# Optimization experiments

Hardware: AMD Instinct MI355X
Metric: run time of the kernel (lower is better)

Reference implementation:

```python
import jax, jax.numpy as jnp
import numpy as np

B, T1, H, P, V = 4096, 65, 64, 50, 32
D = H + P  # input_size = 114


def setup_inputs() -> dict:
    key = jax.random.key(0)
    ks = jax.random.split(key, 20)
    s = 1.0 / np.sqrt(D)
    sh = 1.0 / np.sqrt(H)
    inp = {
        "phonetic_input": jax.random.normal(ks[0], (B, P), dtype=jnp.float32),
        "char_seq": jax.random.randint(ks[1], (B, T1), 0, V, dtype=jnp.int64),
        "emb": jax.random.normal(ks[2], (V, H), dtype=jnp.float32).at[0].set(0.0),  # padding_idx=0
        "W_rx": jax.random.uniform(ks[3], (D, H), jnp.float32, -s, s),
        "b_rx": jax.random.uniform(ks[4], (H,), jnp.float32, -s, s),
        "W_rh": jax.random.uniform(ks[5], (H, H), jnp.float32, -sh, sh),
        "b_rh": jax.random.uniform(ks[6], (H,), jnp.float32, -sh, sh),
        "W_zx": jax.random.uniform(ks[7], (D, H), jnp.float32, -s, s),
        "b_zx": jax.random.uniform(ks[8], (H,), jnp.float32, -s, s),
        "W_zh": jax.random.uniform(ks[9], (H, H), jnp.float32, -sh, sh),
        "b_zh": jax.random.uniform(ks[10], (H,), jnp.float32, -sh, sh),
        "W_hx": jax.random.uniform(ks[11], (D, H), jnp.float32, -s, s),
        "b_hx": jax.random.uniform(ks[12], (H,), jnp.float32, -s, s),
        "W_hh": jax.random.uniform(ks[13], (H, H), jnp.float32, -sh, sh),
        "b_hh": jax.random.uniform(ks[14], (H,), jnp.float32, -sh, sh),
        "W_proj": jax.random.uniform(ks[15], (H, V), jnp.float32, -sh, sh),
        "b_proj": jax.random.uniform(ks[16], (V,), jnp.float32, -sh, sh),
    }
    return inp


def reference(phonetic_input, char_seq, emb, W_rx, b_rx, W_rh, b_rh, W_zx, b_zx,
              W_zh, b_zh, W_hx, b_hx, W_hh, b_hh, W_proj, b_proj):
    input_seq = char_seq[:, :-1]          # [B, T]
    target_seq = char_seq[:, 1:]          # [B, T]
    Bsz, T = input_seq.shape

    char_emb = emb[input_seq]                                   # [B, T, H]
    phon = jnp.broadcast_to(phonetic_input[:, None, :], (Bsz, T, P))
    x = jnp.concatenate([char_emb, phon], axis=2)               # [B, T, D]

    # Hoist input-side projections into batched GEMMs, [T, B, H] for scan
    xr = jnp.einsum('btd,dh->tbh', x, W_rx) + b_rx
    xz = jnp.einsum('btd,dh->tbh', x, W_zx) + b_zx
    xh = jnp.einsum('btd,dh->tbh', x, W_hx) + b_hx

    h0 = jnp.zeros((Bsz, H), dtype=x.dtype)

    def step(h, inputs):
        xr_t, xz_t, xh_t = inputs
        r = jax.nn.sigmoid(xr_t + h @ W_rh + b_rh)
        z = jax.nn.sigmoid(xz_t + h @ W_zh + b_zh)
        c = jnp.tanh(xh_t + (r * h) @ W_hh + b_hh)
        h_new = (1.0 - z) * h + z * c
        return h_new, h_new

    _, hs = jax.lax.scan(step, h0, (xr, xz, xh))                # [T, B, H]
    logits = jnp.einsum('tbh,hv->btv', hs, W_proj) + b_proj     # [B, T, V]

    # cross_entropy with ignore_index=0 (mean over non-ignored)
    targets = target_seq.reshape(-1)
    logp = jax.nn.log_softmax(logits.reshape(-1, V), axis=-1)
    nll = -jnp.take_along_axis(logp, targets[:, None], axis=-1)[:, 0]
    mask = (targets != 0).astype(logits.dtype)
    loss = jnp.sum(nll * mask) / jnp.maximum(jnp.sum(mask), 1.0)
    return logits, loss
```

## Files before the change

### kernel.cpp

```cpp
#include <hip/hip_runtime.h>
#include <stdint.h>

#define Bsz 4096
#define Tn  64
#define T1n 65
#define Hn  64
#define Pn  50
#define Vn  32

typedef __attribute__((ext_vector_type(8))) short short8;
typedef __attribute__((ext_vector_type(4))) float floatx4;

__device__ __forceinline__ float bf2f(unsigned short u) {
  union { unsigned int i; float f; } x; x.i = ((unsigned int)u) << 16; return x.f;
}
__device__ __forceinline__ unsigned short f2bf(float f) {
  union { float f; unsigned int i; } x; x.f = f;
  return (unsigned short)((x.i + 0x7FFFu + ((x.i >> 16) & 1u)) >> 16);
}
__device__ __forceinline__ float fast_sigmoid(float x) {
  return __builtin_amdgcn_rcpf(1.f + __expf(-x));
}
__device__ __forceinline__ float fast_tanh(float x) {
  return 1.f - 2.f * __builtin_amdgcn_rcpf(1.f + __expf(2.f * x));
}

__device__ __forceinline__ short8 load_bfrag(const float* __restrict__ W, int ncols, int col, int kbase) {
  short8 f;
#pragma unroll
  for (int j = 0; j < 8; ++j) f[j] = (short)f2bf(W[(long)(kbase + j) * ncols + col]);
  return f;
}

__launch_bounds__(512)
__global__ void gru_kernel(const float* __restrict__ phon,
                           const int* __restrict__ cs,
                           const float* __restrict__ emb,
                           const float* __restrict__ Wrx, const float* __restrict__ brx,
                           const float* __restrict__ Wrh, const float* __restrict__ brh,
                           const float* __restrict__ Wzx, const float* __restrict__ bzx,
                           const float* __restrict__ Wzh, const float* __restrict__ bzh,
                           const float* __restrict__ Whx, const float* __restrict__ bhx,
                           const float* __restrict__ Whh, const float* __restrict__ bhh,
                           const float* __restrict__ Wpj, const float* __restrict__ bpj_g,
                           float* __restrict__ ws,
                           float* __restrict__ outp) {
  __shared__ unsigned short tbl_s[3 * 32 * 66];
  __shared__ __align__(16) unsigned short hist_s[8 * 1152];
  __shared__ __align__(16) unsigned short rh_s[1152];
  __shared__ __align__(16) float z_cm[64 * 20];
  __shared__ float logit_s[8 * 16 * 33];
  __shared__ unsigned int code4_s[(T1n + 1) * 4];
  __shared__ int det_s[1];
  __shared__ float red_s[16];

  const int tid = threadIdx.x;
  const int b0 = blockIdx.x * 16;
  const int W8 = tid >> 6, lane = tid & 63, q = lane >> 4, c16 = lane & 15;
  const bool isScan = (W8 < 4);
  const int w = isScan ? W8 : (W8 - 4);
  const int jcol = w * 16 + c16;
  const floatx4 zf = {0.f, 0.f, 0.f, 0.f};

  if (tid == 0) det_s[0] = 0;
  __syncthreads();
  if (tid < 128 && cs[2 * tid + 1] != 0) atomicOr(&det_s[0], 1);
  __syncthreads();
  const bool is64 = (det_s[0] == 0);

  for (int i = tid; i < 1152; i += 512) hist_s[7 * 1152 + i] = 0;
  for (int i = tid; i < T1n * 4; i += 512) {
    int t = i >> 2, qq = i & 3;
    unsigned int pk = 0;
#pragma unroll
    for (int r = 0; r < 4; ++r) {
      long idx = (long)(b0 + qq * 4 + r) * T1n + t;
      int c = is64 ? cs[2 * idx] : cs[idx];
      pk |= ((unsigned int)(c & 255)) << (8 * r);
    }
    code4_s[i] = pk;
  }

  for (int g = 0; g < 3; ++g) {
    const float* Wg = (g == 0) ? Wrx : (g == 1) ? Wzx : Whx;
    const float* bx = (g == 0) ? brx : (g == 1) ? bzx : bhx;
    const float* bh = (g == 0) ? brh : (g == 1) ? bzh : bhh;
    float acc[4] = {0.f, 0.f, 0.f, 0.f};
    float bias = bx[lane] + bh[lane];
    for (int d = 0; d < Hn; ++d) {
      float wv = Wg[(long)d * Hn + lane];
#pragma unroll
      for (int k = 0; k < 4; ++k)
        acc[k] += emb[(long)(W8 + 8 * k) * Hn + d] * wv;
    }
#pragma unroll
    for (int k = 0; k < 4; ++k)
      tbl_s[g * 2112 + (W8 + 8 * k) * 66 + lane] = f2bf(acc[k] + bias);
  }

  float ph_a[4] = {0.f, 0.f, 0.f, 0.f};
  float ph_h[4] = {0.f, 0.f, 0.f, 0.f};
  {
    const float* Wa = isScan ? Wrx : Wzx;
    for (int p = 0; p < Pn; ++p) {
      float wa = Wa[(long)(Hn + p) * Hn + jcol];
      float wh = isScan ? Whx[(long)(Hn + p) * Hn + jcol] : 0.f;
#pragma unroll
      for (int r = 0; r < 4; ++r) {
        float xv = phon[(long)(b0 + q * 4 + r) * Pn + p];
        ph_a[r] += xv * wa;
        ph_h[r] += xv * wh;
      }
    }
  }

  short8 Ba0, Ba1;
  short8 Bh0, Bh1;
  short8 Bp0, Bp1;
  float bpj = 0.f;
  {
    const float* Wa = isScan ? Wrh : Wzh;
    Ba0 = load_bfrag(Wa, Hn, jcol, q * 8);
    Ba1 = load_bfrag(Wa, Hn, jcol, 32 + q * 8);
    Bh0 = Ba0; Bh1 = Ba1; Bp0 = Ba0; Bp1 = Ba1;
    if (isScan) {
      Bh0 = load_bfrag(Whh, Hn, jcol, q * 8);
      Bh1 = load_bfrag(Whh, Hn, jcol, 32 + q * 8);
    } else if (W8 < 6) {
      int vt = W8 - 4;
      Bp0 = load_bfrag(Wpj, Vn, vt * 16 + c16, q * 8);
      Bp1 = load_bfrag(Wpj, Vn, vt * 16 + c16, 32 + q * 8);
      bpj = bpj_g[vt * 16 + c16];
    }
  }

  float h[4] = {0.f, 0.f, 0.f, 0.f};
  float nll = 0.f, cnt = 0.f;

  __syncthreads();

  for (int t = 0; t < Tn; ++t) {
    const unsigned int pk = code4_s[t * 4 + q];
    unsigned short tc[4];
    {
      const unsigned short* hp = &hist_s[((t + 7) & 7) * 1152];
      short8 a0 = *(const short8*)&hp[c16 * 72 + q * 8];
      short8 a1 = *(const short8*)&hp[c16 * 72 + 32 + q * 8];
      if (isScan) {
#pragma unroll
        for (int r = 0; r < 4; ++r) {
          int cr = (pk >> (8 * r)) & 255;
          tc[r] = tbl_s[2 * 2112 + cr * 66 + jcol];
        }
      }
      floatx4 acc = __builtin_amdgcn_mfma_f32_16x16x32_bf16(a0, Ba0, zf, 0, 0, 0);
      acc = __builtin_amdgcn_mfma_f32_16x16x32_bf16(a1, Ba1, acc, 0, 0, 0);
      if (isScan) {
#pragma unroll
        for (int r = 0; r < 4; ++r) {
          int cr = (pk >> (8 * r)) & 255;
          float xr = bf2f(tbl_s[0 * 2112 + cr * 66 + jcol]) + ph_a[r] + acc[r];
          rh_s[(q * 4 + r) * 72 + jcol] = f2bf(fast_sigmoid(xr) * h[r]);
        }
      } else {
        floatx4 z4;
#pragma unroll
        for (int r = 0; r < 4; ++r) {
          int cr = (pk >> (8 * r)) & 255;
          float xz = bf2f(tbl_s[1 * 2112 + cr * 66 + jcol]) + ph_a[r] + acc[r];
          z4[r] = fast_sigmoid(xz);
        }
        *(floatx4*)&z_cm[jcol * 20 + q * 4] = z4;
      }
    }
    __syncthreads();

    if (isScan) {
      short8 p0 = *(const short8*)&rh_s[c16 * 72 + q * 8];
      short8 p1 = *(const short8*)&rh_s[c16 * 72 + 32 + q * 8];
      floatx4 z4 = *(const floatx4*)&z_cm[jcol * 20 + q * 4];
      floatx4 acc = __builtin_amdgcn_mfma_f32_16x16x32_bf16(p0, Bh0, zf, 0, 0, 0);
      acc = __builtin_amdgcn_mfma_f32_16x16x32_bf16(p1, Bh1, acc, 0, 0, 0);
      unsigned short* hw = &hist_s[(t & 7) * 1152];
#pragma unroll
      for (int r = 0; r < 4; ++r) {
        float xh = bf2f(tc[r]) + ph_h[r] + acc[r];
        float c = fast_tanh(xh);
        float hn = (1.f - z4[r]) * h[r] + z4[r] * c;
        h[r] = hn;
        hw[(q * 4 + r) * 72 + jcol] = f2bf(hn);
      }
    } else if (W8 < 6) {
      if (t > 0) {
        const unsigned short* hp = &hist_s[((t + 7) & 7) * 1152];
        short8 a0 = *(const short8*)&hp[c16 * 72 + q * 8];
        short8 a1 = *(const short8*)&hp[c16 * 72 + 32 + q * 8];
        floatx4 l = __builtin_amdgcn_mfma_f32_16x16x32_bf16(a0, Bp0, zf, 0, 0, 0);
        l = __builtin_amdgcn_mfma_f32_16x16x32_bf16(a1, Bp1, l, 0, 0, 0);
        float* pg = &logit_s[((t - 1) & 7) * 528];
        int vt = W8 - 4;
#pragma unroll
        for (int r = 0; r < 4; ++r)
          pg[(q * 4 + r) * 33 + vt * 16 + c16] = l[r] + bpj;
      }
    }
    __syncthreads();

    if ((t & 7) == 7) {
      int p = t - 8 + W8;
      if (p >= 0) {
        const float* pg = &logit_s[(p & 7) * 528];
        int v = lane & 31, hf = lane >> 5;
#pragma unroll
        for (int i = 0; i < 8; ++i) {
          int m = i * 2 + hf;
          float lg = pg[m * 33 + v];
          float s = __expf(lg);
#pragma unroll
          for (int off = 16; off >= 1; off >>= 1) s += __shfl_xor(s, off);
          float lse = __logf(s);
          outp[(((long)(b0 + m)) * Tn + p) * Vn + v] = lg;
          unsigned int pk1 = code4_s[(p + 1) * 4 + (m >> 2)];
          int targ = (pk1 >> (8 * (m & 3))) & 255;
          if (targ != 0 && v == targ) { nll += lse - lg; cnt += 1.f; }
        }
      }
    }
  }

  __syncthreads();
  if (W8 >= 4 && W8 < 6) {
    const unsigned short* hp = &hist_s[7 * 1152];
    short8 a0 = *(const short8*)&hp[c16 * 72 + q * 8];
    short8 a1 = *(const short8*)&hp[c16 * 72 + 32 + q * 8];
    floatx4 l = __builtin_amdgcn_mfma_f32_16x16x32_bf16(a0, Bp0, zf, 0, 0, 0);
    l = __builtin_amdgcn_mfma_f32_16x16x32_bf16(a1, Bp1, l, 0, 0, 0);
    int vt = W8 - 4;
#pragma unroll
    for (int r = 0; r < 4; ++r)
      logit_s[7 * 528 + (q * 4 + r) * 33 + vt * 16 + c16] = l[r] + bpj;
  }
  __syncthreads();
  if (W8 == 0) {
    const float* pg = &logit_s[7 * 528];
    int v = lane & 31, hf = lane >> 5;
#pragma unroll
    for (int i = 0; i < 8; ++i) {
      int m = i * 2 + hf;
      float lg = pg[m * 33 + v];
      float s = __expf(lg);
#pragma unroll
      for (int off = 16; off >= 1; off >>= 1) s += __shfl_xor(s, off);
      float lse = __logf(s);
      outp[(((long)(b0 + m)) * Tn + 63) * Vn + v] = lg;
      unsigned int pk1 = code4_s[64 * 4 + (m >> 2)];
      int targ = (pk1 >> (8 * (m & 3))) & 255;
      if (targ != 0 && v == targ) { nll += lse - lg; cnt += 1.f; }
    }
  }

#pragma unroll
  for (int off = 32; off >= 1; off >>= 1) {
    nll += __shfl_xor(nll, off);
    cnt += __shfl_xor(cnt, off);
  }
  if (lane == 0) { red_s[W8] = nll; red_s[8 + W8] = cnt; }
  __syncthreads();
  if (tid == 0) {
    float n = 0.f, c = 0.f;
#pragma unroll
    for (int i = 0; i < 8; ++i) { n += red_s[i]; c += red_s[8 + i]; }
    ws[2 * blockIdx.x] = n;
    ws[2 * blockIdx.x + 1] = c;
  }
}

__global__ void loss_kernel(const float* __restrict__ ws, float* __restrict__ outp) {
  int lane = threadIdx.x;
  float n = 0.f, c = 0.f;
  for (int i = lane; i < Bsz / 16; i += 64) { n += ws[2 * i]; c += ws[2 * i + 1]; }
#pragma unroll
  for (int off = 32; off >= 1; off >>= 1) {
    n += __shfl_xor(n, off);
    c += __shfl_xor(c, off);
  }
  if (lane == 0) outp[(size_t)Bsz * Tn * Vn] = n / fmaxf(c, 1.f);
}

extern "C" void kernel_launch(void* const* d_in, const int* in_sizes, int n_in,
                              void* d_out, int out_size, void* d_ws, size_t ws_size,
                              hipStream_t stream) {
  const float* phon = (const float*)d_in[0];
  const int*   cs   = (const int*)d_in[1];
  const float* emb  = (const float*)d_in[2];
  const float* Wrx  = (const float*)d_in[3];
  const float* brx  = (const float*)d_in[4];
  const float* Wrh  = (const float*)d_in[5];
  const float* brh  = (const float*)d_in[6];
  const float* Wzx  = (const float*)d_in[7];
  const float* bzx  = (const float*)d_in[8];
  const float* Wzh  = (const float*)d_in[9];
  const float* bzh  = (const float*)d_in[10];
  const float* Whx  = (const float*)d_in[11];
  const float* bhx  = (const float*)d_in[12];
  const float* Whh  = (const float*)d_in[13];
  const float* bhh  = (const float*)d_in[14];
  const float* Wpj  = (const float*)d_in[15];
  const float* bpj  = (const float*)d_in[16];
  float* ws = (float*)d_ws;

  hipLaunchKernelGGL(gru_kernel, dim3(Bsz / 16), dim3(512), 0, stream,
                     phon, cs, emb, Wrx, brx, Wrh, brh, Wzx, bzx, Wzh, bzh,
                     Whx, bhx, Whh, bhh, Wpj, bpj, ws, (float*)d_out);
  hipLaunchKernelGGL(loss_kernel, dim3(1), dim3(64), 0, stream, ws, (float*)d_out);
}
```

Measured before the change: 175.6 us.

## Fuse z-gate into scan warps and move projection into first phase

The scan waves now compute both the r and z gate recurrent MFMAs themselves and keep z in registers, which removes the z_cm shared-memory exchange. The logit projection MFMA moves into the first phase of each step, where it overlaps with the gate computation, and the logit ring buffer grows to nine slots so the write slot cannot collide with reads. This puts more work on the scan waves' critical path (four MFMAs instead of two, plus more sigmoids) while idling the former z waves. It also drops a barrier before the tail, and the GRU update becomes a single fma.

```diff
diff --git a/kernel.cpp b/kernel.cpp
--- a/kernel.cpp
+++ b/kernel.cpp
@@ -48,8 +48,7 @@
   __shared__ unsigned short tbl_s[3 * 32 * 66];
   __shared__ __align__(16) unsigned short hist_s[8 * 1152];
   __shared__ __align__(16) unsigned short rh_s[1152];
-  __shared__ __align__(16) float z_cm[64 * 20];
-  __shared__ float logit_s[8 * 16 * 33];
+  __shared__ float logit_s[9 * 16 * 33];
   __shared__ unsigned int code4_s[(T1n + 1) * 4];
   __shared__ int det_s[1];
   __shared__ float red_s[16];
@@ -98,87 +97,89 @@
       tbl_s[g * 2112 + (W8 + 8 * k) * 66 + lane] = f2bf(acc[k] + bias);
   }
 
-  float ph_a[4] = {0.f, 0.f, 0.f, 0.f};
+  float ph_r[4] = {0.f, 0.f, 0.f, 0.f};
+  float ph_z[4] = {0.f, 0.f, 0.f, 0.f};
   float ph_h[4] = {0.f, 0.f, 0.f, 0.f};
-  {
-    const float* Wa = isScan ? Wrx : Wzx;
+  if (isScan) {
     for (int p = 0; p < Pn; ++p) {
-      float wa = Wa[(long)(Hn + p) * Hn + jcol];
-      float wh = isScan ? Whx[(long)(Hn + p) * Hn + jcol] : 0.f;
+      float wr = Wrx[(long)(Hn + p) * Hn + jcol];
+      float wz = Wzx[(long)(Hn + p) * Hn + jcol];
+      float wh = Whx[(long)(Hn + p) * Hn + jcol];
 #pragma unroll
       for (int r = 0; r < 4; ++r) {
         float xv = phon[(long)(b0 + q * 4 + r) * Pn + p];
-        ph_a[r] += xv * wa;
-        ph_h[r] += xv * wh;
+        ph_r[r] += xv * wr; ph_z[r] += xv * wz; ph_h[r] += xv * wh;
       }
     }
   }
 
-  short8 Ba0, Ba1;
-  short8 Bh0, Bh1;
+  short8 Br0, Br1, Bz0, Bz1, Bh0, Bh1;
   short8 Bp0, Bp1;
   float bpj = 0.f;
-  {
-    const float* Wa = isScan ? Wrh : Wzh;
-    Ba0 = load_bfrag(Wa, Hn, jcol, q * 8);
-    Ba1 = load_bfrag(Wa, Hn, jcol, 32 + q * 8);
-    Bh0 = Ba0; Bh1 = Ba1; Bp0 = Ba0; Bp1 = Ba1;
-    if (isScan) {
-      Bh0 = load_bfrag(Whh, Hn, jcol, q * 8);
-      Bh1 = load_bfrag(Whh, Hn, jcol, 32 + q * 8);
-    } else if (W8 < 6) {
-      int vt = W8 - 4;
-      Bp0 = load_bfrag(Wpj, Vn, vt * 16 + c16, q * 8);
-      Bp1 = load_bfrag(Wpj, Vn, vt * 16 + c16, 32 + q * 8);
-      bpj = bpj_g[vt * 16 + c16];
-    }
+  if (isScan) {
+    Br0 = load_bfrag(Wrh, Hn, jcol, q * 8);
+    Br1 = load_bfrag(Wrh, Hn, jcol, 32 + q * 8);
+    Bz0 = load_bfrag(Wzh, Hn, jcol, q * 8);
+    Bz1 = load_bfrag(Wzh, Hn, jcol, 32 + q * 8);
+    Bh0 = load_bfrag(Whh, Hn, jcol, q * 8);
+    Bh1 = load_bfrag(Whh, Hn, jcol, 32 + q * 8);
+    Bp0 = Br0; Bp1 = Br1;
+  } else if (W8 < 6) {
+    int vt = W8 - 4;
+    Bp0 = load_bfrag(Wpj, Vn, vt * 16 + c16, q * 8);
+    Bp1 = load_bfrag(Wpj, Vn, vt * 16 + c16, 32 + q * 8);
+    bpj = bpj_g[vt * 16 + c16];
+    Br0 = Bp0; Br1 = Bp1; Bz0 = Bp0; Bz1 = Bp1; Bh0 = Bp0; Bh1 = Bp1;
+  } else {
+    short8 zs = {0,0,0,0,0,0,0,0};
+    Br0 = zs; Br1 = zs; Bz0 = zs; Bz1 = zs; Bh0 = zs; Bh1 = zs; Bp0 = zs; Bp1 = zs;
   }
 
   float h[4] = {0.f, 0.f, 0.f, 0.f};
+  float z4[4] = {0.f, 0.f, 0.f, 0.f};
   float nll = 0.f, cnt = 0.f;
+  int pp = 0;
 
   __syncthreads();
 
   for (int t = 0; t < Tn; ++t) {
     const unsigned int pk = code4_s[t * 4 + q];
     unsigned short tc[4];
-    {
+    if (isScan) {
       const unsigned short* hp = &hist_s[((t + 7) & 7) * 1152];
       short8 a0 = *(const short8*)&hp[c16 * 72 + q * 8];
       short8 a1 = *(const short8*)&hp[c16 * 72 + 32 + q * 8];
-      if (isScan) {
-#pragma unroll
-        for (int r = 0; r < 4; ++r) {
-          int cr = (pk >> (8 * r)) & 255;
-          tc[r] = tbl_s[2 * 2112 + cr * 66 + jcol];
-        }
+      floatx4 accr = __builtin_amdgcn_mfma_f32_16x16x32_bf16(a0, Br0, zf, 0, 0, 0);
+      floatx4 accz = __builtin_amdgcn_mfma_f32_16x16x32_bf16(a0, Bz0, zf, 0, 0, 0);
+      accr = __builtin_amdgcn_mfma_f32_16x16x32_bf16(a1, Br1, accr, 0, 0, 0);
+      accz = __builtin_amdgcn_mfma_f32_16x16x32_bf16(a1, Bz1, accz, 0, 0, 0);
+#pragma unroll
+      for (int r = 0; r < 4; ++r) {
+        int cr = (pk >> (8 * r)) & 255;
+        tc[r] = tbl_s[2 * 2112 + cr * 66 + jcol];
+        float xr = bf2f(tbl_s[0 * 2112 + cr * 66 + jcol]) + ph_r[r] + accr[r];
+        float xz = bf2f(tbl_s[1 * 2112 + cr * 66 + jcol]) + ph_z[r] + accz[r];
+        z4[r] = fast_sigmoid(xz);
+        rh_s[(q * 4 + r) * 72 + jcol] = f2bf(fast_sigmoid(xr) * h[r]);
       }
-      floatx4 acc = __builtin_amdgcn_mfma_f32_16x16x32_bf16(a0, Ba0, zf, 0, 0, 0);
-      acc = __builtin_amdgcn_mfma_f32_16x16x32_bf16(a1, Ba1, acc, 0, 0, 0);
-      if (isScan) {
-#pragma unroll
-        for (int r = 0; r < 4; ++r) {
-          int cr = (pk >> (8 * r)) & 255;
-          float xr = bf2f(tbl_s[0 * 2112 + cr * 66 + jcol]) + ph_a[r] + acc[r];
-          rh_s[(q * 4 + r) * 72 + jcol] = f2bf(fast_sigmoid(xr) * h[r]);
-        }
-      } else {
-        floatx4 z4;
-#pragma unroll
-        for (int r = 0; r < 4; ++r) {
-          int cr = (pk >> (8 * r)) & 255;
-          float xz = bf2f(tbl_s[1 * 2112 + cr * 66 + jcol]) + ph_a[r] + acc[r];
-          z4[r] = fast_sigmoid(xz);
-        }
-        *(floatx4*)&z_cm[jcol * 20 + q * 4] = z4;
-      }
+    } else if (W8 < 6 && t > 0) {
+      const unsigned short* hp = &hist_s[((t + 7) & 7) * 1152];
+      short8 a0 = *(const short8*)&hp[c16 * 72 + q * 8];
+      short8 a1 = *(const short8*)&hp[c16 * 72 + 32 + q * 8];
+      floatx4 l = __builtin_amdgcn_mfma_f32_16x16x32_bf16(a0, Bp0, zf, 0, 0, 0);
+      l = __builtin_amdgcn_mfma_f32_16x16x32_bf16(a1, Bp1, l, 0, 0, 0);
+      float* pg = &logit_s[pp * 528];
+      int vt = W8 - 4;
+#pragma unroll
+      for (int r = 0; r < 4; ++r)
+        pg[(q * 4 + r) * 33 + vt * 16 + c16] = l[r] + bpj;
+      pp = (pp == 8) ? 0 : pp + 1;
     }
     __syncthreads();
 
     if (isScan) {
       short8 p0 = *(const short8*)&rh_s[c16 * 72 + q * 8];
       short8 p1 = *(const short8*)&rh_s[c16 * 72 + 32 + q * 8];
-      floatx4 z4 = *(const floatx4*)&z_cm[jcol * 20 + q * 4];
       floatx4 acc = __builtin_amdgcn_mfma_f32_16x16x32_bf16(p0, Bh0, zf, 0, 0, 0);
       acc = __builtin_amdgcn_mfma_f32_16x16x32_bf16(p1, Bh1, acc, 0, 0, 0);
       unsigned short* hw = &hist_s[(t & 7) * 1152];
@@ -186,30 +187,17 @@
       for (int r = 0; r < 4; ++r) {
         float xh = bf2f(tc[r]) + ph_h[r] + acc[r];
         float c = fast_tanh(xh);
-        float hn = (1.f - z4[r]) * h[r] + z4[r] * c;
+        float hn = fmaf(z4[r], c - h[r], h[r]);
         h[r] = hn;
         hw[(q * 4 + r) * 72 + jcol] = f2bf(hn);
       }
-    } else if (W8 < 6) {
-      if (t > 0) {
-        const unsigned short* hp = &hist_s[((t + 7) & 7) * 1152];
-        short8 a0 = *(const short8*)&hp[c16 * 72 + q * 8];
-        short8 a1 = *(const short8*)&hp[c16 * 72 + 32 + q * 8];
-        floatx4 l = __builtin_amdgcn_mfma_f32_16x16x32_bf16(a0, Bp0, zf, 0, 0, 0);
-        l = __builtin_amdgcn_mfma_f32_16x16x32_bf16(a1, Bp1, l, 0, 0, 0);
-        float* pg = &logit_s[((t - 1) & 7) * 528];
-        int vt = W8 - 4;
-#pragma unroll
-        for (int r = 0; r < 4; ++r)
-          pg[(q * 4 + r) * 33 + vt * 16 + c16] = l[r] + bpj;
-      }
     }
     __syncthreads();
 
     if ((t & 7) == 7) {
       int p = t - 8 + W8;
       if (p >= 0) {
-        const float* pg = &logit_s[(p & 7) * 528];
+        const float* pg = &logit_s[(p % 9) * 528];
         int v = lane & 31, hf = lane >> 5;
 #pragma unroll
         for (int i = 0; i < 8; ++i) {
@@ -228,7 +216,6 @@
     }
   }
 
-  __syncthreads();
   if (W8 >= 4 && W8 < 6) {
     const unsigned short* hp = &hist_s[7 * 1152];
     short8 a0 = *(const short8*)&hp[c16 * 72 + q * 8];
@@ -238,11 +225,11 @@
     int vt = W8 - 4;
 #pragma unroll
     for (int r = 0; r < 4; ++r)
-      logit_s[7 * 528 + (q * 4 + r) * 33 + vt * 16 + c16] = l[r] + bpj;
+      logit_s[0 * 528 + (q * 4 + r) * 33 + vt * 16 + c16] = l[r] + bpj;
   }
   __syncthreads();
   if (W8 == 0) {
-    const float* pg = &logit_s[7 * 528];
+    const float* pg = &logit_s[0 * 528];
     int v = lane & 31, hf = lane >> 5;
 #pragma unroll
     for (int i = 0; i < 8; ++i) {
```

Measured after the change: 170.8 us. 1.03x faster.
